# Kernel optimization log

Measured on AMD Instinct MI355X. Metric: run time of the kernel, lower is better.

The kernel has to match this reference:

```python
import jax, jax.numpy as jnp
import numpy as np

B, S, D = 4, 2048, 1024
H = 16
HD = D // H
DFF = 4096
MAX_REL = 32
EPS = 1e-5


def _rms_norm(x, w):
    rms = jnp.sqrt(jnp.mean(x * x, axis=-1, keepdims=True) + EPS)
    return x / rms * w


def setup_inputs() -> dict:
    key = jax.random.key(0)
    ks = jax.random.split(key, 16)
    sc = 0.02
    d = {
        "x": jax.random.normal(ks[0], (B, S, D), dtype=jnp.float32),
        "g1": jnp.ones((D,), dtype=jnp.float32),
        "g2": jnp.ones((D,), dtype=jnp.float32),
        "wq": jax.random.normal(ks[1], (D, D), dtype=jnp.float32) * sc,
        "bq": jnp.zeros((D,), dtype=jnp.float32),
        "wk": jax.random.normal(ks[2], (D, D), dtype=jnp.float32) * sc,
        "bk": jnp.zeros((D,), dtype=jnp.float32),
        "wv": jax.random.normal(ks[3], (D, D), dtype=jnp.float32) * sc,
        "bv": jnp.zeros((D,), dtype=jnp.float32),
        "wo": jax.random.normal(ks[4], (D, D), dtype=jnp.float32) * sc,
        "bo": jnp.zeros((D,), dtype=jnp.float32),
        "rel_pos": jax.random.normal(ks[5], (H, 2 * MAX_REL + 1), dtype=jnp.float32),
        "w1": jax.random.normal(ks[6], (D, DFF), dtype=jnp.float32) * sc,
        "b1": jnp.zeros((DFF,), dtype=jnp.float32),
        "w2": jax.random.normal(ks[7], (DFF, D), dtype=jnp.float32) * sc,
        "b2": jnp.zeros((D,), dtype=jnp.float32),
    }
    return d


def reference(x, g1, g2, wq, bq, wk, bk, wv, bv, wo, bo, rel_pos, w1, b1, w2, b2):
    b, s, d = x.shape
    # --- multi-head attention with relative-position bias ---
    q = (x @ wq + bq).reshape(b, s, H, HD).transpose(0, 2, 1, 3)  # [B,H,S,HD]
    k = (x @ wk + bk).reshape(b, s, H, HD).transpose(0, 2, 1, 3)
    v = (x @ wv + bv).reshape(b, s, H, HD).transpose(0, 2, 1, 3)
    scores = jnp.einsum("bhqd,bhkd->bhqk", q, k) / jnp.sqrt(jnp.float32(HD))
    # relative position bias: gather from (H, 2*MAX_REL+1) table
    pos = jnp.arange(s)
    rel = pos[None, :] - pos[:, None]                # [S,S]
    idx = jnp.clip(rel, -MAX_REL, MAX_REL) + MAX_REL  # [S,S]
    bias = rel_pos[:, idx]                            # [H,S,S]
    scores = scores + bias[None]
    attn = jax.nn.softmax(scores, axis=-1)
    out = jnp.einsum("bhqk,bhkd->bhqd", attn, v)
    out = out.transpose(0, 2, 1, 3).reshape(b, s, d)
    attn_out = out @ wo + bo
    # residual + RMSNorm
    x = _rms_norm(attn_out + x, g1)
    # --- feed-forward (exact GELU) ---
    h = jax.nn.gelu(x @ w1 + b1, approximate=False)
    ff = h @ w2 + b2
    x = _rms_norm(ff + x, g2)
    return x
```

## Files before the change

kernel.cpp:

```cpp
#include <hip/hip_runtime.h>

#define B_ 4
#define S_ 2048
#define D_ 1024
#define H_ 16
#define HD_ 64
#define DFF_ 4096
#define MR_ 32
#define M_ (B_*S_)

typedef unsigned short u16;
typedef __attribute__((ext_vector_type(8))) short bf16x8;
typedef __attribute__((ext_vector_type(4))) float f32x4;

#define MFMA16 __builtin_amdgcn_mfma_f32_16x16x32_bf16
#define A_CONST 0.18033688011112f
#define LOG2E_ 1.44269504088896f

__device__ __forceinline__ u16 f2b(float f) {
  unsigned u = __builtin_bit_cast(unsigned, f);
  u = u + 0x7FFFu + ((u >> 16) & 1u);
  return (u16)(u >> 16);
}
__device__ __forceinline__ float b2f(u16 h) {
  unsigned u = ((unsigned)h) << 16;
  return __builtin_bit_cast(float, u);
}
__device__ __forceinline__ float exp2_fast(float x) {
  float r;
  asm("v_exp_f32 %0, %1" : "=v"(r) : "v"(x));
  return r;
}
__device__ __forceinline__ unsigned cvtpk(float lo, float hi) {
  unsigned r;
  asm("v_cvt_pk_bf16_f32 %0, %1, %2" : "=v"(r) : "v"(lo), "v"(hi));
  return r;
}
__device__ __forceinline__ int med3i(int a, int b, int c) {
  int r;
  asm("v_med3_i32 %0, %1, %2, %3" : "=v"(r) : "v"(a), "v"(b), "v"(c));
  return r;
}
__device__ __forceinline__ float gelu_t(float v) {
  float v2 = v * v;
  float z  = v * fmaf(v2, 0.1029394f, 2.3021171f);
  float e  = exp2_fast(z);
  float r;
  asm("v_rcp_f32 %0, %1" : "=v"(r) : "v"(e + 1.0f));
  return v - v * r;
}
__device__ __forceinline__ void gl_lds16(const void* g, void* l) {
  __builtin_amdgcn_global_load_lds(
      (const __attribute__((address_space(1))) void*)g,
      (__attribute__((address_space(3))) void*)l, 16, 0, 0);
}

#define SWZ(r) ((((((r)>>3)&1)<<2) ^ ((r)&7)) << 4)
#define SWZ64(r) ((((r)>>1)&3) << 4)

__global__ __launch_bounds__(256) void prep_kernel(
    const float* __restrict__ x, u16* __restrict__ xb,
    const float* __restrict__ wq, const float* __restrict__ wk,
    const float* __restrict__ wv, const float* __restrict__ wo,
    const float* __restrict__ w1, const float* __restrict__ w2,
    u16* __restrict__ wqT, u16* __restrict__ wkT, u16* __restrict__ wvT,
    u16* __restrict__ woT, u16* __restrict__ w1T, u16* __restrict__ w2T)
{
  int bid = blockIdx.x;
  const int tid = threadIdx.x;
  if (bid < 8192) {
    int i = bid * 256 + tid;
    float4 v = ((const float4*)x)[i];
    ushort4 o;
    o.x = f2b(v.x); o.y = f2b(v.y); o.z = f2b(v.z); o.w = f2b(v.w);
    ((ushort4*)xb)[i] = o;
    return;
  }
  bid -= 8192;
  const float* in; u16* out; int R, C, local;
  if (bid < 4096) {
    int m = bid >> 10;
    in  = m == 0 ? wq  : (m == 1 ? wk  : (m == 2 ? wv  : wo));
    out = m == 0 ? wqT : (m == 1 ? wkT : (m == 2 ? wvT : woT));
    R = 1024; C = 1024; local = bid & 1023;
  } else if (bid < 8192) {
    in = w1; out = w1T; R = 1024; C = 4096; local = bid - 4096;
  } else {
    in = w2; out = w2T; R = 4096; C = 1024; local = bid - 8192;
  }
  const int ctiles = C >> 5;
  const int c0 = (local % ctiles) * 32;
  const int r0 = (local / ctiles) * 32;
  const int xx = tid & 31, yy = tid >> 5;
  __shared__ float t[32][33];
#pragma unroll
  for (int i = 0; i < 4; ++i)
    t[yy + i*8][xx] = in[(long)(r0 + yy + i*8) * C + c0 + xx];
  __syncthreads();
#pragma unroll
  for (int i = 0; i < 4; ++i)
    out[(long)(c0 + yy + i*8) * R + r0 + xx] = f2b(t[xx][yy + i*8]);
}

__global__ __launch_bounds__(256) void vtrans_kernel(const u16* __restrict__ v,
                                                     u16* __restrict__ vT) {
  __shared__ u16 t[32][33];
  int bh = blockIdx.y; int b = bh >> 4, h = bh & 15;
  int s0 = (blockIdx.x >> 1) * 32;
  int d0 = (blockIdx.x & 1) * 32;
  int x = threadIdx.x, y = threadIdx.y;
#pragma unroll
  for (int i = 0; i < 4; ++i)
    t[y + i*8][x] = v[((long)(b*S_ + s0 + y + i*8)) * D_ + h*64 + d0 + x];
  __syncthreads();
#pragma unroll
  for (int i = 0; i < 4; ++i)
    vT[((long)((b*H_ + h)*HD_ + d0 + y + i*8)) * S_ + s0 + x] = t[x][y + i*8];
}

template<int EPI, int WN>
__global__ __launch_bounds__(512, 2) void gemm10(
    const u16* __restrict__ A, const u16* __restrict__ BT,
    const float* __restrict__ bias0, const float* __restrict__ bias1,
    const float* __restrict__ bias2,
    u16* __restrict__ C0, u16* __restrict__ C1, u16* __restrict__ C2,
    int Ndim, int Kdim)
{
  constexpr int BM = (WN == 4) ? 128 : 256;
  constexpr int BN = WN * 64;
  constexpr int SLOT = (BM + BN) * 64;
  __shared__ char lds[3 * SLOT];
  const int tid = threadIdx.x;
  const int w = tid >> 6, lane = tid & 63;
  const int lr = lane & 15, lg = lane >> 4;
  const int wm = w / WN, wn = w % WN;

  const int nbx = Ndim / BN;
  const int cpx = gridDim.x >> 3;
  const int bid = blockIdx.x;
  const int swzb = (bid & 7) * cpx + (bid >> 3);
  const long blockM = (long)(swzb / nbx) * BM;
  const long blockN = (long)(swzb % nbx) * BN;

  const int srow = tid >> 2;
  const int scol = ((tid & 3) * 16) ^ SWZ64(srow);
  const u16* Ag  = A  + (blockM + srow) * (long)Kdim + (scol >> 1);
  const u16* Ag2 = Ag + (long)128 * Kdim;
  const u16* Bg  = BT + (blockN + srow) * (long)Kdim + (scol >> 1);
  const u16* Bg2 = Bg + (long)128 * Kdim;

  auto STAGE = [&](int slot, long ko) {
    char* base = &lds[slot * SLOT];
    gl_lds16(Ag + ko, base + w * 1024);
    if constexpr (WN == 2) gl_lds16(Ag2 + ko, base + 8192 + w * 1024);
    gl_lds16(Bg + ko, base + BM * 64 + w * 1024);
    if constexpr (WN == 4) gl_lds16(Bg2 + ko, base + BM * 64 + 8192 + w * 1024);
  };

  const int rsw = (lg * 16) ^ SWZ64(lr);
  int offA[4], offB[4];
#pragma unroll
  for (int mf = 0; mf < 4; ++mf) offA[mf] = (wm*64 + mf*16 + lr) * 64 + rsw;
#pragma unroll
  for (int nf = 0; nf < 4; ++nf) offB[nf] = BM*64 + (wn*64 + nf*16 + lr) * 64 + rsw;

  f32x4 acc[4][4] = {};
  const int NS = Kdim >> 5;

  STAGE(0, 0);
  STAGE(1, 32);
  asm volatile("s_waitcnt vmcnt(3)" ::: "memory");
  __builtin_amdgcn_s_barrier();

  int sl = 0, sl2 = 2;
  for (int t = 0; t < NS; ++t) {
    const char* s = &lds[sl * SLOT];
    bf16x8 af[4], bfr[4];
#pragma unroll
    for (int mf = 0; mf < 4; ++mf) af[mf] = *(const bf16x8*)(s + offA[mf]);
#pragma unroll
    for (int nf = 0; nf < 4; ++nf) bfr[nf] = *(const bf16x8*)(s + offB[nf]);
    if (t + 2 < NS) {
      STAGE(sl2, (long)(t + 2) * 32);
      asm volatile("s_waitcnt vmcnt(3)" ::: "memory");
    } else if (t == NS - 2) {
      asm volatile("s_waitcnt vmcnt(0)" ::: "memory");
    }
    __builtin_amdgcn_s_barrier();
    __builtin_amdgcn_s_setprio(1);
#pragma unroll
    for (int mf = 0; mf < 4; ++mf)
#pragma unroll
      for (int nf = 0; nf < 4; ++nf)
        acc[mf][nf] = MFMA16(bfr[nf], af[mf], acc[mf][nf], 0, 0, 0);
    __builtin_amdgcn_s_setprio(0);
    __builtin_amdgcn_s_barrier();
    sl  = (sl  == 2) ? 0 : sl  + 1;
    sl2 = (sl2 == 2) ? 0 : sl2 + 1;
  }

  const float* bsel = bias0;
  u16* osel = C0;
  long nstride = Ndim;
  long ncol0 = blockN;
  if (EPI == 3) {
    int mat = (int)(blockN >> 10);
    bsel = mat == 0 ? bias0 : (mat == 1 ? bias1 : bias2);
    osel = mat == 0 ? C0 : (mat == 1 ? C1 : C2);
    nstride = 1024;
    ncol0 = blockN & 1023;
  }
  constexpr int RB = BN * 2;
  char* const et = &lds[0];
#pragma unroll
  for (int mf = 0; mf < 4; ++mf) {
    const int row = wm*64 + mf*16 + lr;
#pragma unroll
    for (int nf = 0; nf < 4; ++nf) {
      const int colu = wn*64 + nf*16 + lg*4;
      float4 bv = *(const float4*)&bsel[ncol0 + colu];
      float v0 = acc[mf][nf][0] + bv.x;
      float v1 = acc[mf][nf][1] + bv.y;
      float v2 = acc[mf][nf][2] + bv.z;
      float v3 = acc[mf][nf][3] + bv.w;
      if (EPI == 2) {
        v0 = gelu_t(v0); v1 = gelu_t(v1); v2 = gelu_t(v2); v3 = gelu_t(v3);
      }
      ushort4 st;
      st.x = f2b(v0); st.y = f2b(v1); st.z = f2b(v2); st.w = f2b(v3);
      *(ushort4*)(et + row*RB + ((colu*2) ^ ((row & 7) << 4))) = st;
    }
  }
  __syncthreads();
  constexpr int CHR  = RB / 16;
  constexpr int ITER = BM * CHR / 512;
#pragma unroll
  for (int i = 0; i < ITER; ++i) {
    const int idx = i*512 + tid;
    const int row = idx / CHR;
    const int cb  = (idx % CHR) * 16;
    uint4 val = *(const uint4*)(et + row*RB + (cb ^ ((row & 7) << 4)));
    *(uint4*)&osel[(blockM + row) * nstride + ncol0 + (cb >> 1)] = val;
  }
}

__device__ __forceinline__ void packp(const float* p, bf16x8* pfo) {
#pragma unroll
  for (int ks = 0; ks < 2; ++ks) {
    uint4 uu;
    uu.x = cvtpk(p[ks*4+0], p[ks*4+1]);
    uu.y = cvtpk(p[ks*4+2], p[ks*4+3]);
    uu.z = cvtpk(p[(ks+2)*4+0], p[(ks+2)*4+1]);
    uu.w = cvtpk(p[(ks+2)*4+2], p[(ks+2)*4+3]);
    pfo[ks] = __builtin_bit_cast(bf16x8, uu);
  }
}

__device__ __forceinline__ void sm_uni(const f32x4* s, float bu, bf16x8* pfo) {
  float p[16];
#pragma unroll
  for (int ni = 0; ni < 4; ++ni)
#pragma unroll
    for (int j = 0; j < 4; ++j)
      p[ni*4+j] = exp2_fast(fmaf(s[ni][j], A_CONST, bu));
  packp(p, pfo);
}

__device__ __forceinline__ void sm_slow(const f32x4* s, const float* relb,
                                        int rbase, bf16x8* pfo) {
  float p[16];
#pragma unroll
  for (int ni = 0; ni < 4; ++ni) {
    const int koff = (ni&1)*32 + (ni>>1)*4;
#pragma unroll
    for (int j = 0; j < 4; ++j) {
      int idx = med3i(rbase + koff + j + MR_, 0, 2*MR_);
      p[ni*4+j] = exp2_fast(fmaf(s[ni][j], A_CONST, relb[idx]));
    }
  }
  packp(p, pfo);
}

__global__ __launch_bounds__(256, 4) void attn5_kernel(
    const u16* __restrict__ q, const u16* __restrict__ k,
    const u16* __restrict__ vT, const float* __restrict__ rel_pos,
    u16* __restrict__ ao)
{
  __shared__ u16 KB[2][4096];
  __shared__ u16 VB[2][4096];
  __shared__ float relb[2*MR_ + 1];

  const int tid = threadIdx.x;
  const int w = tid >> 6, lane = tid & 63;
  const int lr = lane & 15, lg = lane >> 4;
  const int qt = blockIdx.x, bh = blockIdx.y;
  const int b = bh >> 4, h = bh & 15;
  const int q0 = qt * 128;
  const int qq = q0 + w*32;

  if (tid < 2*MR_ + 1) relb[tid] = rel_pos[h * (2*MR_ + 1) + tid] * LOG2E_;

  const int srow0 = w*8 + (lane >> 3);
  const int srow1 = 32 + srow0;
  const int scb   = (lane & 7) * 16;
  const int col0  = scb ^ SWZ(srow0);
  const int col1  = scb ^ SWZ(srow1);

  const long qkbase = ((long)(b*S_)) * D_ + h*64;
  const long vbase  = ((long)((b*H_ + h) * HD_)) * S_;

  {
    const u16* qg = q + qkbase + (long)q0 * D_;
#pragma unroll
    for (int c = 0; c < 4; ++c) {
      int row = c*32 + srow0;
      int colc = scb ^ SWZ(row);
      gl_lds16(qg + (long)row*D_ + (colc >> 1), &KB[0][0] + (c*32 + w*8)*64);
    }
  }
  __syncthreads();
  bf16x8 qf[4];
#pragma unroll
  for (int qi = 0; qi < 2; ++qi)
#pragma unroll
    for (int ks = 0; ks < 2; ++ks) {
      int row = w*32 + qi*16 + lr;
      qf[qi*2+ks] = *(const bf16x8*)((const char*)&KB[0][0] + row*128 + ((ks*64 + lg*16) ^ SWZ(row)));
    }
  const float bHI = relb[2*MR_];
  const float bLO = relb[0];
  __syncthreads();

  int offK0[4], offV0[4];
#pragma unroll
  for (int ni = 0; ni < 4; ++ni) {
    int kr = (ni&1)*32 + (lr>>2)*8 + (ni>>1)*4 + (lr&3);
    int vr = ni*16 + lr;
    offK0[ni] = kr*128 + ((lg*16) ^ SWZ(kr));
    offV0[ni] = vr*128 + ((lg*16) ^ SWZ(vr));
  }

  const u16* kp0 = k  + qkbase + (long)srow0*D_ + (col0 >> 1);
  const u16* kp1 = k  + qkbase + (long)srow1*D_ + (col1 >> 1);
  const u16* vp0 = vT + vbase  + (long)srow0*S_ + (col0 >> 1);
  const u16* vp1 = vT + vbase  + (long)srow1*S_ + (col1 >> 1);
  u16* kb_w0 = &KB[0][(w*8)*64];
  u16* kb_w1 = &KB[0][(32 + w*8)*64];
  u16* vb_w0 = &VB[0][(w*8)*64];
  u16* vb_w1 = &VB[0][(32 + w*8)*64];

  bf16x8 onesf;
#pragma unroll
  for (int i = 0; i < 8; ++i) onesf[i] = (short)0x3F80;

  f32x4 acco[2][4] = {};
  f32x4 accl[2] = {};

  gl_lds16(kp0, kb_w0);
  gl_lds16(kp1, kb_w1);
  gl_lds16(vp0, vb_w0);
  gl_lds16(vp1, vb_w1);

  const long kstep = (long)64 * D_;
  const int NT = S_ / 64;
  for (int t = 0; t < NT; ++t) {
    const int cur = t & 1;
    __syncthreads();
    if (t + 1 < NT) {
      int bufo = (cur ^ 1) * 4096;
      gl_lds16(kp0 + (long)(t+1)*kstep, kb_w0 + bufo);
      gl_lds16(kp1 + (long)(t+1)*kstep, kb_w1 + bufo);
      gl_lds16(vp0 + (t+1)*64, vb_w0 + bufo);
      gl_lds16(vp1 + (t+1)*64, vb_w1 + bufo);
    }
    const char* Kb = (const char*)&KB[cur][0];
    const char* Vb = (const char*)&VB[cur][0];
    const int k0 = t * 64;

    f32x4 s0[4] = {}, s1[4] = {};
#pragma unroll
    for (int ks = 0; ks < 2; ++ks)
#pragma unroll
      for (int ni = 0; ni < 4; ++ni) {
        bf16x8 kf = *(const bf16x8*)(Kb + (offK0[ni] ^ (ks*64)));
        s0[ni] = MFMA16(kf, qf[ks],   s0[ni], 0, 0, 0);
        s1[ni] = MFMA16(kf, qf[2+ks], s1[ni], 0, 0, 0);
      }

    bf16x8 pf0[2], pf1[2];
    bool hi_u = (k0 - (qq + 31)) >= MR_;
    bool lo_u = (qq - (k0 + 63)) >= MR_;
    if (hi_u || lo_u) {
      float bu = hi_u ? bHI : bLO;
      sm_uni(s0, bu, pf0);
      sm_uni(s1, bu, pf1);
    } else {
      int rb0 = k0 + lg*8 - (qq + lr);
      sm_slow(s0, relb, rb0,      pf0);
      sm_slow(s1, relb, rb0 - 16, pf1);
    }

#pragma unroll
    for (int ks = 0; ks < 2; ++ks) {
#pragma unroll
      for (int ni = 0; ni < 4; ++ni) {
        bf16x8 vf = *(const bf16x8*)(Vb + (offV0[ni] ^ (ks*64)));
        acco[0][ni] = MFMA16(vf, pf0[ks], acco[0][ni], 0, 0, 0);
        acco[1][ni] = MFMA16(vf, pf1[ks], acco[1][ni], 0, 0, 0);
      }
      accl[0] = MFMA16(onesf, pf0[ks], accl[0], 0, 0, 0);
      accl[1] = MFMA16(onesf, pf1[ks], accl[1], 0, 0, 0);
    }
  }

#pragma unroll
  for (int qi = 0; qi < 2; ++qi) {
    float inv = 1.0f / accl[qi][0];
    long orow = ((long)(b*S_ + qq + qi*16 + lr)) * D_ + h*64;
#pragma unroll
    for (int ni = 0; ni < 4; ++ni) {
      ushort4 ov;
      ov.x = f2b(acco[qi][ni][0] * inv);
      ov.y = f2b(acco[qi][ni][1] * inv);
      ov.z = f2b(acco[qi][ni][2] * inv);
      ov.w = f2b(acco[qi][ni][3] * inv);
      *(ushort4*)(ao + orow + ni*16 + lg*4) = ov;
    }
  }
}

template<int ABF, int BBF>
__global__ __launch_bounds__(256) void rmsnorm_kernel(
    const void* __restrict__ a, const void* __restrict__ b,
    const float* __restrict__ g, float* __restrict__ outf,
    u16* __restrict__ outb)
{
  long row = blockIdx.x;
  int tid = threadIdx.x;
  float ya[4], yb[4], y[4];
  if (ABF) {
    ushort4 av = ((const ushort4*)a)[row*256 + tid];
    ya[0] = b2f(av.x); ya[1] = b2f(av.y); ya[2] = b2f(av.z); ya[3] = b2f(av.w);
  } else {
    float4 av = ((const float4*)a)[row*256 + tid];
    ya[0] = av.x; ya[1] = av.y; ya[2] = av.z; ya[3] = av.w;
  }
  if (BBF) {
    ushort4 bv = ((const ushort4*)b)[row*256 + tid];
    yb[0] = b2f(bv.x); yb[1] = b2f(bv.y); yb[2] = b2f(bv.z); yb[3] = b2f(bv.w);
  } else {
    float4 bv = ((const float4*)b)[row*256 + tid];
    yb[0] = bv.x; yb[1] = bv.y; yb[2] = bv.z; yb[3] = bv.w;
  }
  float ss = 0.f;
#pragma unroll
  for (int i = 0; i < 4; ++i) { y[i] = ya[i] + yb[i]; ss += y[i]*y[i]; }
#pragma unroll
  for (int m = 1; m < 64; m <<= 1) ss += __shfl_xor(ss, m);
  __shared__ float red[4];
  int w = tid >> 6, lane = tid & 63;
  if (lane == 0) red[w] = ss;
  __syncthreads();
  ss = red[0] + red[1] + red[2] + red[3];
  float rinv = rsqrtf(ss * (1.0f / D_) + 1e-5f);
  float4 gv = ((const float4*)g)[tid];
  float o[4] = { y[0]*rinv*gv.x, y[1]*rinv*gv.y, y[2]*rinv*gv.z, y[3]*rinv*gv.w };
  if (outf) {
    float4 of = { o[0], o[1], o[2], o[3] };
    ((float4*)outf)[row*256 + tid] = of;
  }
  if (outb) {
    ushort4 ob;
    ob.x = f2b(o[0]); ob.y = f2b(o[1]); ob.z = f2b(o[2]); ob.w = f2b(o[3]);
    ((ushort4*)outb)[row*256 + tid] = ob;
  }
}

extern "C" void kernel_launch(void* const* d_in, const int* in_sizes, int n_in,
                              void* d_out, int out_size, void* d_ws, size_t ws_size,
                              hipStream_t stream) {
  const float* x   = (const float*)d_in[0];
  const float* g1  = (const float*)d_in[1];
  const float* g2  = (const float*)d_in[2];
  const float* wq  = (const float*)d_in[3];
  const float* bq  = (const float*)d_in[4];
  const float* wk  = (const float*)d_in[5];
  const float* bk  = (const float*)d_in[6];
  const float* wv  = (const float*)d_in[7];
  const float* bv  = (const float*)d_in[8];
  const float* wo  = (const float*)d_in[9];
  const float* bo  = (const float*)d_in[10];
  const float* rel = (const float*)d_in[11];
  const float* w1  = (const float*)d_in[12];
  const float* b1  = (const float*)d_in[13];
  const float* w2  = (const float*)d_in[14];
  const float* b2  = (const float*)d_in[15];
  float* out = (float*)d_out;

  char* ws = (char*)d_ws;
  const size_t MB = 1024ull * 1024ull;
  u16* xb   = (u16*)(ws + 0);
  u16* wqT  = (u16*)(ws + 16*MB);
  u16* wkT  = (u16*)(ws + 18*MB);
  u16* wvT  = (u16*)(ws + 20*MB);
  u16* woT  = (u16*)(ws + 22*MB);
  u16* w1T  = (u16*)(ws + 24*MB);
  u16* w2T  = (u16*)(ws + 32*MB);
  u16* qb   = (u16*)(ws + 40*MB);
  u16* kb   = (u16*)(ws + 56*MB);
  u16* vb   = (u16*)(ws + 72*MB);
  u16* vTb  = (u16*)(ws + 88*MB);
  u16* aob  = (u16*)(ws + 104*MB);
  u16* prjb = (u16*)(ws + 120*MB);
  u16* x1b  = (u16*)(ws + 136*MB);
  u16* hb   = (u16*)(ws + 40*MB);
  u16* ffb  = (u16*)(ws + 120*MB);
  (void)ws_size; (void)in_sizes; (void)n_in; (void)out_size;

  prep_kernel<<<20480, 256, 0, stream>>>(
      x, xb, wq, wk, wv, wo, w1, w2, wqT, wkT, wvT, woT, w1T, w2T);

  gemm10<3,4><<<(3072/256)*(M_/128), 512, 0, stream>>>(
      xb, wqT, bq, bk, bv, qb, kb, vb, 3072, D_);

  vtrans_kernel<<<dim3((S_/32)*(HD_/32), B_*H_), dim3(32, 8), 0, stream>>>(vb, vTb);

  attn5_kernel<<<dim3(S_/128, B_*H_), 256, 0, stream>>>(qb, kb, vTb, rel, aob);

  gemm10<0,2><<<(D_/128)*(M_/256), 512, 0, stream>>>(
      aob, woT, bo, nullptr, nullptr, prjb, nullptr, nullptr, D_, D_);

  rmsnorm_kernel<1,1><<<M_, 256, 0, stream>>>(prjb, xb, g1, nullptr, x1b);

  gemm10<2,4><<<(DFF_/256)*(M_/128), 512, 0, stream>>>(
      x1b, w1T, b1, nullptr, nullptr, hb, nullptr, nullptr, DFF_, D_);

  gemm10<0,2><<<(D_/128)*(M_/256), 512, 0, stream>>>(
      hb, w2T, b2, nullptr, nullptr, ffb, nullptr, nullptr, D_, DFF_);

  rmsnorm_kernel<1,1><<<M_, 256, 0, stream>>>(ffb, x1b, g2, out, nullptr);
}
```

Measured before the change: 408.0 us.

## Enlarge attention query tile to 64 rows per warp for more K/V reuse

New measurement: 386.9 us. 5.2% less time.

```diff
diff --git a/kernel.cpp b/kernel.cpp
--- a/kernel.cpp
+++ b/kernel.cpp
@@ -281,13 +281,12 @@
   packp(p, pfo);
 }
 
-__global__ __launch_bounds__(256, 4) void attn5_kernel(
+__global__ __launch_bounds__(256, 2) void attn7_kernel(
     const u16* __restrict__ q, const u16* __restrict__ k,
     const u16* __restrict__ vT, const float* __restrict__ rel_pos,
     u16* __restrict__ ao)
 {
-  __shared__ u16 KB[2][4096];
-  __shared__ u16 VB[2][4096];
+  __shared__ u16 SM[16384];
   __shared__ float relb[2*MR_ + 1];
 
   const int tid = threadIdx.x;
@@ -295,8 +294,8 @@
   const int lr = lane & 15, lg = lane >> 4;
   const int qt = blockIdx.x, bh = blockIdx.y;
   const int b = bh >> 4, h = bh & 15;
-  const int q0 = qt * 128;
-  const int qq = q0 + w*32;
+  const int q0 = qt * 256;
+  const int qlo = q0 + w*64;
 
   if (tid < 2*MR_ + 1) relb[tid] = rel_pos[h * (2*MR_ + 1) + tid] * LOG2E_;
 
@@ -312,20 +311,17 @@
   {
     const u16* qg = q + qkbase + (long)q0 * D_;
 #pragma unroll
-    for (int c = 0; c < 4; ++c) {
-      int row = c*32 + srow0;
-      int colc = scb ^ SWZ(row);
-      gl_lds16(qg + (long)row*D_ + (colc >> 1), &KB[0][0] + (c*32 + w*8)*64);
-    }
+    for (int c = 0; c < 8; ++c)
+      gl_lds16(qg + (long)(c*32 + srow0)*D_ + (col0 >> 1), &SM[(c*32 + w*8)*64]);
   }
   __syncthreads();
-  bf16x8 qf[4];
-#pragma unroll
-  for (int qi = 0; qi < 2; ++qi)
+  bf16x8 qf[4][2];
+#pragma unroll
+  for (int qi = 0; qi < 4; ++qi)
 #pragma unroll
     for (int ks = 0; ks < 2; ++ks) {
-      int row = w*32 + qi*16 + lr;
-      qf[qi*2+ks] = *(const bf16x8*)((const char*)&KB[0][0] + row*128 + ((ks*64 + lg*16) ^ SWZ(row)));
+      int row = w*64 + qi*16 + lr;
+      qf[qi][ks] = *(const bf16x8*)((const char*)&SM[0] + row*128 + ((ks*64 + lg*16) ^ SWZ(row)));
     }
   const float bHI = relb[2*MR_];
   const float bLO = relb[0];
@@ -344,17 +340,17 @@
   const u16* kp1 = k  + qkbase + (long)srow1*D_ + (col1 >> 1);
   const u16* vp0 = vT + vbase  + (long)srow0*S_ + (col0 >> 1);
   const u16* vp1 = vT + vbase  + (long)srow1*S_ + (col1 >> 1);
-  u16* kb_w0 = &KB[0][(w*8)*64];
-  u16* kb_w1 = &KB[0][(32 + w*8)*64];
-  u16* vb_w0 = &VB[0][(w*8)*64];
-  u16* vb_w1 = &VB[0][(32 + w*8)*64];
+  u16* kb_w0 = &SM[(w*8)*64];
+  u16* kb_w1 = &SM[(32 + w*8)*64];
+  u16* vb_w0 = &SM[8192 + (w*8)*64];
+  u16* vb_w1 = &SM[8192 + (32 + w*8)*64];
 
   bf16x8 onesf;
 #pragma unroll
   for (int i = 0; i < 8; ++i) onesf[i] = (short)0x3F80;
 
-  f32x4 acco[2][4] = {};
-  f32x4 accl[2] = {};
+  f32x4 acco[4][4] = {};
+  f32x4 accl[4] = {};
 
   gl_lds16(kp0, kb_w0);
   gl_lds16(kp1, kb_w1);
@@ -373,31 +369,32 @@
       gl_lds16(vp0 + (t+1)*64, vb_w0 + bufo);
       gl_lds16(vp1 + (t+1)*64, vb_w1 + bufo);
     }
-    const char* Kb = (const char*)&KB[cur][0];
-    const char* Vb = (const char*)&VB[cur][0];
+    const char* Kb = (const char*)&SM[cur * 4096];
+    const char* Vb = (const char*)&SM[8192 + cur * 4096];
     const int k0 = t * 64;
 
-    f32x4 s0[4] = {}, s1[4] = {};
+    f32x4 sc[4][4] = {};
 #pragma unroll
     for (int ks = 0; ks < 2; ++ks)
 #pragma unroll
       for (int ni = 0; ni < 4; ++ni) {
         bf16x8 kf = *(const bf16x8*)(Kb + (offK0[ni] ^ (ks*64)));
-        s0[ni] = MFMA16(kf, qf[ks],   s0[ni], 0, 0, 0);
-        s1[ni] = MFMA16(kf, qf[2+ks], s1[ni], 0, 0, 0);
+#pragma unroll
+        for (int qi = 0; qi < 4; ++qi)
+          sc[qi][ni] = MFMA16(kf, qf[qi][ks], sc[qi][ni], 0, 0, 0);
       }
 
-    bf16x8 pf0[2], pf1[2];
-    bool hi_u = (k0 - (qq + 31)) >= MR_;
-    bool lo_u = (qq - (k0 + 63)) >= MR_;
+    bf16x8 pf[4][2];
+    bool hi_u = (k0 - (qlo + 63)) >= MR_;
+    bool lo_u = (qlo - (k0 + 63)) >= MR_;
     if (hi_u || lo_u) {
       float bu = hi_u ? bHI : bLO;
-      sm_uni(s0, bu, pf0);
-      sm_uni(s1, bu, pf1);
+#pragma unroll
+      for (int qi = 0; qi < 4; ++qi) sm_uni(sc[qi], bu, pf[qi]);
     } else {
-      int rb0 = k0 + lg*8 - (qq + lr);
-      sm_slow(s0, relb, rb0,      pf0);
-      sm_slow(s1, relb, rb0 - 16, pf1);
+      int rb0 = k0 + lg*8 - (qlo + lr);
+#pragma unroll
+      for (int qi = 0; qi < 4; ++qi) sm_slow(sc[qi], relb, rb0 - qi*16, pf[qi]);
     }
 
 #pragma unroll
@@ -405,18 +402,20 @@
 #pragma unroll
       for (int ni = 0; ni < 4; ++ni) {
         bf16x8 vf = *(const bf16x8*)(Vb + (offV0[ni] ^ (ks*64)));
-        acco[0][ni] = MFMA16(vf, pf0[ks], acco[0][ni], 0, 0, 0);
-        acco[1][ni] = MFMA16(vf, pf1[ks], acco[1][ni], 0, 0, 0);
+#pragma unroll
+        for (int qi = 0; qi < 4; ++qi)
+          acco[qi][ni] = MFMA16(vf, pf[qi][ks], acco[qi][ni], 0, 0, 0);
       }
-      accl[0] = MFMA16(onesf, pf0[ks], accl[0], 0, 0, 0);
-      accl[1] = MFMA16(onesf, pf1[ks], accl[1], 0, 0, 0);
-    }
-  }
-
-#pragma unroll
-  for (int qi = 0; qi < 2; ++qi) {
+#pragma unroll
+      for (int qi = 0; qi < 4; ++qi)
+        accl[qi] = MFMA16(onesf, pf[qi][ks], accl[qi], 0, 0, 0);
+    }
+  }
+
+#pragma unroll
+  for (int qi = 0; qi < 4; ++qi) {
     float inv = 1.0f / accl[qi][0];
-    long orow = ((long)(b*S_ + qq + qi*16 + lr)) * D_ + h*64;
+    long orow = ((long)(b*S_ + qlo + qi*16 + lr)) * D_ + h*64;
 #pragma unroll
     for (int ni = 0; ni < 4; ++ni) {
       ushort4 ov;
@@ -525,7 +524,7 @@
 
   vtrans_kernel<<<dim3((S_/32)*(HD_/32), B_*H_), dim3(32, 8), 0, stream>>>(vb, vTb);
 
-  attn5_kernel<<<dim3(S_/128, B_*H_), 256, 0, stream>>>(qb, kb, vTb, rel, aob);
+  attn7_kernel<<<dim3(S_/256, B_*H_), 256, 0, stream>>>(qb, kb, vTb, rel, aob);
 
   gemm10<0,2><<<(D_/128)*(M_/256), 512, 0, stream>>>(
       aob, woT, bo, nullptr, nullptr, prjb, nullptr, nullptr, D_, D_);
```
